# Optimization experiments

Hardware: AMD Instinct MI355X
Metric: run time of the kernel (lower is better)

## Reference

```python
import jax, jax.numpy as jnp
import numpy as np

N_NODES = 10000
N_EDGES = 320000
NEG_SLOPE = 0.2  # PyG GATConv default leaky_relu slope
EPS = 1e-16      # PyG softmax denominator epsilon


def setup_inputs() -> dict:
    key = jax.random.key(0)
    ks = jax.random.split(key, 9)
    x = jax.random.normal(ks[0], (N_NODES, 128), dtype=jnp.float32)
    edge_index = jax.random.randint(ks[1], (2, N_EDGES), 0, N_NODES, dtype=jnp.int64)
    W1 = jax.random.normal(ks[2], (128, 320), dtype=jnp.float32) * 0.05
    att_src1 = jax.random.normal(ks[3], (5, 64), dtype=jnp.float32) * 0.1
    att_dst1 = jax.random.normal(ks[4], (5, 64), dtype=jnp.float32) * 0.1
    b1 = jnp.zeros((320,), dtype=jnp.float32)
    W2 = jax.random.normal(ks[5], (320, 64), dtype=jnp.float32) * 0.05
    att_src2 = jax.random.normal(ks[6], (1, 64), dtype=jnp.float32) * 0.1
    att_dst2 = jax.random.normal(ks[7], (1, 64), dtype=jnp.float32) * 0.1
    b2 = jnp.zeros((64,), dtype=jnp.float32)
    return {"x": x, "edge_index": edge_index, "W1": W1, "att_src1": att_src1,
            "att_dst1": att_dst1, "b1": b1, "W2": W2, "att_src2": att_src2,
            "att_dst2": att_dst2, "b2": b2}


def gat_conv(x, src, dst, W, att_src, att_dst, bias, heads, out_c, concat):
    """PyG-style GATConv (eval mode, self-loops already in src/dst)."""
    N = x.shape[0]
    h = (x @ W).reshape(N, heads, out_c)                 # [N, H, C]
    a_src = jnp.einsum('nhc,hc->nh', h, att_src)         # [N, H]
    a_dst = jnp.einsum('nhc,hc->nh', h, att_dst)         # [N, H]
    e = a_src[src] + a_dst[dst]                          # [E, H]
    e = jax.nn.leaky_relu(e, NEG_SLOPE)
    # segment softmax over incoming edges of each destination node
    m = jax.ops.segment_max(e, dst, num_segments=N)      # [N, H]
    ex = jnp.exp(e - m[dst])
    s = jax.ops.segment_sum(ex, dst, num_segments=N)     # [N, H]
    alpha = ex / (s[dst] + EPS)                          # [E, H]
    out = jax.ops.segment_sum(h[src] * alpha[:, :, None], dst, num_segments=N)
    if concat:
        out = out.reshape(N, heads * out_c)
    else:
        out = out.mean(axis=1)
    return out + bias


def reference(x, edge_index, W1, att_src1, att_dst1, b1, W2, att_src2, att_dst2, b2):
    N = x.shape[0]
    loop = jnp.arange(N, dtype=edge_index.dtype)
    src = jnp.concatenate([edge_index[0], loop])  # add self-loops (PyG default)
    dst = jnp.concatenate([edge_index[1], loop])
    h = jax.nn.relu(gat_conv(x, src, dst, W1, att_src1, att_dst1, b1, 5, 64, True))
    h = jax.nn.relu(gat_conv(h, src, dst, W2, att_src2, att_dst2, b2, 1, 64, False))
    # F.dropout with training=False is identity (eval mode)
    return h
```

## Files before the change

kernel.cpp:

```cpp
#include <hip/hip_runtime.h>
#include <math.h>

#define N_NODES 10000
#define N_EDGES 320000
#define ET (N_EDGES + N_NODES)
#define CAP 128
#define NB_G1 (157 * 5)
#define NB_SCT ((ET + 255) / 256)

__device__ __forceinline__ float lrelu_exp(float e) {
  e = (e > 0.f) ? e : 0.2f * e;
  return __expf(e);
}


__global__ __launch_bounds__(256) void k_init(int* __restrict__ cursor) {
  int i = blockIdx.x * 256 + threadIdx.x;
  if (i < N_NODES) cursor[i] = 0;
}


__global__ __launch_bounds__(256) void k_gemm1_scatter(const float* __restrict__ x, const float* __restrict__ W1,
                                                       const float* __restrict__ att_src, const float* __restrict__ att_dst,
                                                       float* __restrict__ h1, float* __restrict__ a_src,
                                                       float* __restrict__ a_dst,
                                                       const int* __restrict__ ei, int* __restrict__ cursor,
                                                       int* __restrict__ csr) {
  __shared__ float xs[128][65];
  int bid = blockIdx.x;
  int t = threadIdx.x;
  if (bid >= NB_G1) {
    int i = (bid - NB_G1) * 256 + t;
    if (i < ET) {
      int src, dst;
      if (i < N_EDGES) { src = ei[i]; dst = ei[N_EDGES + i]; }
      else             { src = dst = i - N_EDGES; }
      int pos = (dst << 7) + atomicAdd(&cursor[dst], 1);
      csr[pos] = src;
    }
    return;
  }
  int h = bid / 157;
  int rb = (bid % 157) * 64;
#pragma unroll
  for (int i = 0; i < 8; ++i) {
    int idx = t + 256 * i;
    int kq = (idx & 31) * 4;
    int row = idx >> 5;
    int gr = rb + row;
    float4 v = make_float4(0.f, 0.f, 0.f, 0.f);
    if (gr < N_NODES) v = *reinterpret_cast<const float4*>(&x[(size_t)gr * 128 + kq]);
    xs[kq + 0][row] = v.x; xs[kq + 1][row] = v.y; xs[kq + 2][row] = v.z; xs[kq + 3][row] = v.w;
  }
  __syncthreads();
  int cg = t & 15, rg = t >> 4;
  int c0 = cg * 4, r0 = rg * 4;
  const float* __restrict__ wp = W1 + h * 64 + c0;
  float4 a0 = make_float4(0.f,0.f,0.f,0.f), a1 = a0, a2 = a0, a3 = a0;
#pragma unroll 4
  for (int k = 0; k < 128; ++k) {
    float4 xv = *reinterpret_cast<const float4*>(&xs[k][r0]);
    float4 wv = *reinterpret_cast<const float4*>(&wp[(size_t)k * 320]);
    a0.x = fmaf(xv.x, wv.x, a0.x); a0.y = fmaf(xv.x, wv.y, a0.y); a0.z = fmaf(xv.x, wv.z, a0.z); a0.w = fmaf(xv.x, wv.w, a0.w);
    a1.x = fmaf(xv.y, wv.x, a1.x); a1.y = fmaf(xv.y, wv.y, a1.y); a1.z = fmaf(xv.y, wv.z, a1.z); a1.w = fmaf(xv.y, wv.w, a1.w);
    a2.x = fmaf(xv.z, wv.x, a2.x); a2.y = fmaf(xv.z, wv.y, a2.y); a2.z = fmaf(xv.z, wv.z, a2.z); a2.w = fmaf(xv.z, wv.w, a2.w);
    a3.x = fmaf(xv.w, wv.x, a3.x); a3.y = fmaf(xv.w, wv.y, a3.y); a3.z = fmaf(xv.w, wv.z, a3.z); a3.w = fmaf(xv.w, wv.w, a3.w);
  }
  float4 asv = *reinterpret_cast<const float4*>(&att_src[h * 64 + c0]);
  float4 adv = *reinterpret_cast<const float4*>(&att_dst[h * 64 + c0]);
#pragma unroll
  for (int rr = 0; rr < 4; ++rr) {
    float4 ar = (rr == 0) ? a0 : (rr == 1) ? a1 : (rr == 2) ? a2 : a3;
    float vs = ar.x * asv.x + ar.y * asv.y + ar.z * asv.z + ar.w * asv.w;
    float vd = ar.x * adv.x + ar.y * adv.y + ar.z * adv.z + ar.w * adv.w;
#pragma unroll
    for (int m = 1; m < 16; m <<= 1) { vs += __shfl_xor(vs, m); vd += __shfl_xor(vd, m); }
    int gr = rb + r0 + rr;
    if (gr < N_NODES) {
      if (cg == 0) { a_src[h * N_NODES + gr] = vs; a_dst[h * N_NODES + gr] = vd; }
      *reinterpret_cast<float4*>(&h1[(size_t)gr * 320 + h * 64 + c0]) = ar;
    }
  }
}


__global__ __launch_bounds__(256) void k_agg1(const float* __restrict__ h1, const float* __restrict__ a_src,
                                              const float* __restrict__ a_dst, const float* __restrict__ b1,
                                              const int* __restrict__ degs, const int* __restrict__ csr,
                                              float* __restrict__ out1) {
  int lane = threadIdx.x & 63, wid = threadIdx.x >> 6;
  int n = blockIdx.x * 4 + wid;
  int h = blockIdx.y;
  int sub = lane >> 4;
  int cq = lane & 15;
  int beg = n << 7;
  int deg = degs[n];
  int limit = beg + deg;
  int end = beg + ((deg + 15) & ~15);
  const float* __restrict__ as = a_src + (size_t)h * N_NODES;
  float adn = a_dst[(size_t)h * N_NODES + n];
  const float* __restrict__ hh = h1 + h * 64 + cq * 4;
  float4 acc = make_float4(0.f, 0.f, 0.f, 0.f);
  float s = 0.f;
  int e = beg + sub;
  bool va = e < limit, vb = e + 4 < limit, vc = e + 8 < limit, vd = e + 12 < limit;
  int t0 = csr[e], t1 = csr[e + 4], t2 = csr[e + 8], t3 = csr[e + 12];
  unsigned i0 = va ? (unsigned)t0 : 0u, i1 = vb ? (unsigned)t1 : 0u;
  unsigned i2 = vc ? (unsigned)t2 : 0u, i3 = vd ? (unsigned)t3 : 0u;
  float v0 = as[i0], v1 = as[i1], v2 = as[i2], v3 = as[i3];
  for (;;) {
    float4 ga = *reinterpret_cast<const float4*>(hh + i0 * 320u);
    float4 gb = *reinterpret_cast<const float4*>(hh + i1 * 320u);
    float4 gc = *reinterpret_cast<const float4*>(hh + i2 * 320u);
    float4 gd = *reinterpret_cast<const float4*>(hh + i3 * 320u);
    float pa = va ? lrelu_exp(v0 + adn) : 0.f;
    float pb = vb ? lrelu_exp(v1 + adn) : 0.f;
    float pc = vc ? lrelu_exp(v2 + adn) : 0.f;
    float pd = vd ? lrelu_exp(v3 + adn) : 0.f;
    e += 16;
    bool more = e < end;
    if (more) {
      va = e < limit; vb = e + 4 < limit; vc = e + 8 < limit; vd = e + 12 < limit;
      t0 = csr[e]; t1 = csr[e + 4]; t2 = csr[e + 8]; t3 = csr[e + 12];
      i0 = va ? (unsigned)t0 : 0u; i1 = vb ? (unsigned)t1 : 0u;
      i2 = vc ? (unsigned)t2 : 0u; i3 = vd ? (unsigned)t3 : 0u;
      v0 = as[i0]; v1 = as[i1]; v2 = as[i2]; v3 = as[i3];
    }
    s += (pa + pb) + (pc + pd);
    acc.x = fmaf(pd, gd.x, fmaf(pc, gc.x, fmaf(pb, gb.x, fmaf(pa, ga.x, acc.x))));
    acc.y = fmaf(pd, gd.y, fmaf(pc, gc.y, fmaf(pb, gb.y, fmaf(pa, ga.y, acc.y))));
    acc.z = fmaf(pd, gd.z, fmaf(pc, gc.z, fmaf(pb, gb.z, fmaf(pa, ga.z, acc.z))));
    acc.w = fmaf(pd, gd.w, fmaf(pc, gc.w, fmaf(pb, gb.w, fmaf(pa, ga.w, acc.w))));
    if (!more) break;
  }
#pragma unroll
  for (int m = 16; m <= 32; m <<= 1) {
    acc.x += __shfl_xor(acc.x, m);
    acc.y += __shfl_xor(acc.y, m);
    acc.z += __shfl_xor(acc.z, m);
    acc.w += __shfl_xor(acc.w, m);
    s += __shfl_xor(s, m);
  }
  if (sub == 0) {
    float inv = 1.f / (s + 1e-16f);
    const float* bp = b1 + h * 64 + cq * 4;
    float4 o;
    o.x = fmaxf(fmaf(acc.x, inv, bp[0]), 0.f);
    o.y = fmaxf(fmaf(acc.y, inv, bp[1]), 0.f);
    o.z = fmaxf(fmaf(acc.z, inv, bp[2]), 0.f);
    o.w = fmaxf(fmaf(acc.w, inv, bp[3]), 0.f);
    *reinterpret_cast<float4*>(&out1[(size_t)n * 320 + h * 64 + cq * 4]) = o;
  }
}

__global__ __launch_bounds__(256) void k_agg2(const float* __restrict__ h2, const float* __restrict__ a_src,
                                              const float* __restrict__ a_dst, const float* __restrict__ b2,
                                              const int* __restrict__ degs, const int* __restrict__ csr,
                                              float* __restrict__ out) {
  int lane = threadIdx.x & 63, wid = threadIdx.x >> 6;
  int n = blockIdx.x * 4 + wid;
  int sub = lane >> 4;
  int cq = lane & 15;
  int beg = n << 7;
  int deg = degs[n];
  int limit = beg + deg;
  int end = beg + ((deg + 15) & ~15);
  float adn = a_dst[n];
  const float* __restrict__ hh = h2 + cq * 4;
  float4 acc = make_float4(0.f, 0.f, 0.f, 0.f);
  float s = 0.f;
  int e = beg + sub;
  bool va = e < limit, vb = e + 4 < limit, vc = e + 8 < limit, vd = e + 12 < limit;
  int t0 = csr[e], t1 = csr[e + 4], t2 = csr[e + 8], t3 = csr[e + 12];
  unsigned i0 = va ? (unsigned)t0 : 0u, i1 = vb ? (unsigned)t1 : 0u;
  unsigned i2 = vc ? (unsigned)t2 : 0u, i3 = vd ? (unsigned)t3 : 0u;
  float v0 = a_src[i0], v1 = a_src[i1], v2 = a_src[i2], v3 = a_src[i3];
  for (;;) {
    float4 ga = *reinterpret_cast<const float4*>(hh + i0 * 64u);
    float4 gb = *reinterpret_cast<const float4*>(hh + i1 * 64u);
    float4 gc = *reinterpret_cast<const float4*>(hh + i2 * 64u);
    float4 gd = *reinterpret_cast<const float4*>(hh + i3 * 64u);
    float pa = va ? lrelu_exp(v0 + adn) : 0.f;
    float pb = vb ? lrelu_exp(v1 + adn) : 0.f;
    float pc = vc ? lrelu_exp(v2 + adn) : 0.f;
    float pd = vd ? lrelu_exp(v3 + adn) : 0.f;
    e += 16;
    bool more = e < end;
    if (more) {
      va = e < limit; vb = e + 4 < limit; vc = e + 8 < limit; vd = e + 12 < limit;
      t0 = csr[e]; t1 = csr[e + 4]; t2 = csr[e + 8]; t3 = csr[e + 12];
      i0 = va ? (unsigned)t0 : 0u; i1 = vb ? (unsigned)t1 : 0u;
      i2 = vc ? (unsigned)t2 : 0u; i3 = vd ? (unsigned)t3 : 0u;
      v0 = a_src[i0]; v1 = a_src[i1]; v2 = a_src[i2]; v3 = a_src[i3];
    }
    s += (pa + pb) + (pc + pd);
    acc.x = fmaf(pd, gd.x, fmaf(pc, gc.x, fmaf(pb, gb.x, fmaf(pa, ga.x, acc.x))));
    acc.y = fmaf(pd, gd.y, fmaf(pc, gc.y, fmaf(pb, gb.y, fmaf(pa, ga.y, acc.y))));
    acc.z = fmaf(pd, gd.z, fmaf(pc, gc.z, fmaf(pb, gb.z, fmaf(pa, ga.z, acc.z))));
    acc.w = fmaf(pd, gd.w, fmaf(pc, gc.w, fmaf(pb, gb.w, fmaf(pa, ga.w, acc.w))));
    if (!more) break;
  }
#pragma unroll
  for (int m = 16; m <= 32; m <<= 1) {
    acc.x += __shfl_xor(acc.x, m);
    acc.y += __shfl_xor(acc.y, m);
    acc.z += __shfl_xor(acc.z, m);
    acc.w += __shfl_xor(acc.w, m);
    s += __shfl_xor(s, m);
  }
  if (sub == 0) {
    float inv = 1.f / (s + 1e-16f);
    const float* bp = b2 + cq * 4;
    float4 o;
    o.x = fmaxf(fmaf(acc.x, inv, bp[0]), 0.f);
    o.y = fmaxf(fmaf(acc.y, inv, bp[1]), 0.f);
    o.z = fmaxf(fmaf(acc.z, inv, bp[2]), 0.f);
    o.w = fmaxf(fmaf(acc.w, inv, bp[3]), 0.f);
    *reinterpret_cast<float4*>(&out[(size_t)n * 64 + cq * 4]) = o;
  }
}


__global__ __launch_bounds__(256) void k_gemm2(const float* __restrict__ out1, const float* __restrict__ W2,
                                               float* __restrict__ h2part) {
  __shared__ float xs[64][65];
  int t = threadIdx.x;
  int rb = blockIdx.x * 64;
  int kc = blockIdx.y;
#pragma unroll
  for (int i = 0; i < 4; ++i) {
    int idx = t + 256 * i;
    int kq = (idx & 15) * 4;
    int row = idx >> 4;
    int gr = rb + row;
    float4 v = make_float4(0.f, 0.f, 0.f, 0.f);
    if (gr < N_NODES) v = *reinterpret_cast<const float4*>(&out1[(size_t)gr * 320 + kc * 64 + kq]);
    xs[kq + 0][row] = v.x; xs[kq + 1][row] = v.y; xs[kq + 2][row] = v.z; xs[kq + 3][row] = v.w;
  }
  __syncthreads();
  int cg = t & 15, rg = t >> 4;
  int c0 = cg * 4, r0 = rg * 4;
  const float* __restrict__ wp = W2 + (size_t)kc * 64 * 64 + c0;
  float4 a0 = make_float4(0.f,0.f,0.f,0.f), a1 = a0, a2 = a0, a3 = a0;
#pragma unroll 4
  for (int k = 0; k < 64; ++k) {
    float4 xv = *reinterpret_cast<const float4*>(&xs[k][r0]);
    float4 wv = *reinterpret_cast<const float4*>(&wp[(size_t)k * 64]);
    a0.x = fmaf(xv.x, wv.x, a0.x); a0.y = fmaf(xv.x, wv.y, a0.y); a0.z = fmaf(xv.x, wv.z, a0.z); a0.w = fmaf(xv.x, wv.w, a0.w);
    a1.x = fmaf(xv.y, wv.x, a1.x); a1.y = fmaf(xv.y, wv.y, a1.y); a1.z = fmaf(xv.y, wv.z, a1.z); a1.w = fmaf(xv.y, wv.w, a1.w);
    a2.x = fmaf(xv.z, wv.x, a2.x); a2.y = fmaf(xv.z, wv.y, a2.y); a2.z = fmaf(xv.z, wv.z, a2.z); a2.w = fmaf(xv.z, wv.w, a2.w);
    a3.x = fmaf(xv.w, wv.x, a3.x); a3.y = fmaf(xv.w, wv.y, a3.y); a3.z = fmaf(xv.w, wv.z, a3.z); a3.w = fmaf(xv.w, wv.w, a3.w);
  }
  float* __restrict__ hp = h2part + (size_t)kc * N_NODES * 64;
#pragma unroll
  for (int rr = 0; rr < 4; ++rr) {
    float4 ar = (rr == 0) ? a0 : (rr == 1) ? a1 : (rr == 2) ? a2 : a3;
    int gr = rb + r0 + rr;
    if (gr < N_NODES) *reinterpret_cast<float4*>(&hp[(size_t)gr * 64 + c0]) = ar;
  }
}


__global__ __launch_bounds__(256) void k_hred2(const float* __restrict__ h2part,
                                               const float* __restrict__ att_src, const float* __restrict__ att_dst,
                                               float* __restrict__ h2, float* __restrict__ a_src,
                                               float* __restrict__ a_dst) {
  int n = blockIdx.x * 4 + (threadIdx.x >> 6);
  int c = threadIdx.x & 63;
  if (n >= N_NODES) return;
  float v = 0.f;
#pragma unroll
  for (int kc = 0; kc < 5; ++kc) v += h2part[((size_t)kc * N_NODES + n) * 64 + c];
  float vs = v * att_src[c], vd = v * att_dst[c];
  for (int off = 32; off; off >>= 1) {
    vs += __shfl_down(vs, off);
    vd += __shfl_down(vd, off);
  }
  h2[(size_t)n * 64 + c] = v;
  if (c == 0) { a_src[n] = vs; a_dst[n] = vd; }
}


extern "C" void kernel_launch(void* const* d_in, const int* in_sizes, int n_in,
                              void* d_out, int out_size, void* d_ws, size_t ws_size,
                              hipStream_t stream) {
  (void)in_sizes; (void)n_in; (void)out_size; (void)ws_size;
  const float* x    = (const float*)d_in[0];
  const int*   ei   = (const int*)d_in[1];
  const float* W1   = (const float*)d_in[2];
  const float* as1w = (const float*)d_in[3];
  const float* ad1w = (const float*)d_in[4];
  const float* b1   = (const float*)d_in[5];
  const float* W2   = (const float*)d_in[6];
  const float* as2w = (const float*)d_in[7];
  const float* ad2w = (const float*)d_in[8];
  const float* b2   = (const float*)d_in[9];
  float* out = (float*)d_out;

  char* ws = (char*)d_ws;
  size_t off = 0;
  auto alloc = [&](size_t bytes) -> void* {
    void* p = ws + off;
    off += (bytes + 255) & ~(size_t)255;
    return p;
  };
  float*  h1     = (float*)alloc((size_t)N_NODES * 320 * 4);
  float*  out1   = (float*)alloc((size_t)N_NODES * 320 * 4);
  float*  h2     = (float*)alloc((size_t)N_NODES * 64 * 4);
  float*  h2part = (float*)alloc((size_t)5 * N_NODES * 64 * 4);
  float*  a_src1 = (float*)alloc((size_t)5 * N_NODES * 4);
  float*  a_dst1 = (float*)alloc((size_t)5 * N_NODES * 4);
  float*  a_src2 = (float*)alloc((size_t)N_NODES * 4);
  float*  a_dst2 = (float*)alloc((size_t)N_NODES * 4);
  int*    cursor = (int*)alloc((size_t)N_NODES * 4);
  int*    csr    = (int*)alloc((size_t)N_NODES * CAP * 4);

  k_init<<<(N_NODES + 255) / 256, 256, 0, stream>>>(cursor);
  k_gemm1_scatter<<<NB_G1 + NB_SCT, 256, 0, stream>>>(x, W1, as1w, ad1w, h1, a_src1, a_dst1,
                                                      ei, cursor, csr);
  {
    dim3 g(N_NODES / 4, 5);
    k_agg1 <<<g, 256, 0, stream>>>(h1, a_src1, a_dst1, b1, cursor, csr, out1);
  }
  {
    dim3 g((N_NODES + 63) / 64, 5);
    k_gemm2<<<g, 256, 0, stream>>>(out1, W2, h2part);
  }
  k_hred2<<<(N_NODES + 3) / 4, 256, 0, stream>>>(h2part, as2w, ad2w, h2, a_src2, a_dst2);
  k_agg2 <<<N_NODES / 4, 256, 0, stream>>>(h2, a_src2, a_dst2, b2, cursor, csr, out);
}
```

Measured before the change: 103.4 us.

## Fuse second-layer GEMM with attention-score reduction, dropping split-K partials

```diff
diff --git a/kernel.cpp b/kernel.cpp
--- a/kernel.cpp
+++ b/kernel.cpp
@@ -222,62 +222,44 @@
 
 
 __global__ __launch_bounds__(256) void k_gemm2(const float* __restrict__ out1, const float* __restrict__ W2,
-                                               float* __restrict__ h2part) {
-  __shared__ float xs[64][65];
-  int t = threadIdx.x;
-  int rb = blockIdx.x * 64;
-  int kc = blockIdx.y;
-#pragma unroll
-  for (int i = 0; i < 4; ++i) {
-    int idx = t + 256 * i;
-    int kq = (idx & 15) * 4;
-    int row = idx >> 4;
-    int gr = rb + row;
-    float4 v = make_float4(0.f, 0.f, 0.f, 0.f);
-    if (gr < N_NODES) v = *reinterpret_cast<const float4*>(&out1[(size_t)gr * 320 + kc * 64 + kq]);
-    xs[kq + 0][row] = v.x; xs[kq + 1][row] = v.y; xs[kq + 2][row] = v.z; xs[kq + 3][row] = v.w;
-  }
-  __syncthreads();
-  int cg = t & 15, rg = t >> 4;
-  int c0 = cg * 4, r0 = rg * 4;
-  const float* __restrict__ wp = W2 + (size_t)kc * 64 * 64 + c0;
-  float4 a0 = make_float4(0.f,0.f,0.f,0.f), a1 = a0, a2 = a0, a3 = a0;
-#pragma unroll 4
-  for (int k = 0; k < 64; ++k) {
-    float4 xv = *reinterpret_cast<const float4*>(&xs[k][r0]);
-    float4 wv = *reinterpret_cast<const float4*>(&wp[(size_t)k * 64]);
-    a0.x = fmaf(xv.x, wv.x, a0.x); a0.y = fmaf(xv.x, wv.y, a0.y); a0.z = fmaf(xv.x, wv.z, a0.z); a0.w = fmaf(xv.x, wv.w, a0.w);
-    a1.x = fmaf(xv.y, wv.x, a1.x); a1.y = fmaf(xv.y, wv.y, a1.y); a1.z = fmaf(xv.y, wv.z, a1.z); a1.w = fmaf(xv.y, wv.w, a1.w);
-    a2.x = fmaf(xv.z, wv.x, a2.x); a2.y = fmaf(xv.z, wv.y, a2.y); a2.z = fmaf(xv.z, wv.z, a2.z); a2.w = fmaf(xv.z, wv.w, a2.w);
-    a3.x = fmaf(xv.w, wv.x, a3.x); a3.y = fmaf(xv.w, wv.y, a3.y); a3.z = fmaf(xv.w, wv.z, a3.z); a3.w = fmaf(xv.w, wv.w, a3.w);
-  }
-  float* __restrict__ hp = h2part + (size_t)kc * N_NODES * 64;
-#pragma unroll
-  for (int rr = 0; rr < 4; ++rr) {
-    float4 ar = (rr == 0) ? a0 : (rr == 1) ? a1 : (rr == 2) ? a2 : a3;
-    int gr = rb + r0 + rr;
-    if (gr < N_NODES) *reinterpret_cast<float4*>(&hp[(size_t)gr * 64 + c0]) = ar;
-  }
-}
-
-
-__global__ __launch_bounds__(256) void k_hred2(const float* __restrict__ h2part,
                                                const float* __restrict__ att_src, const float* __restrict__ att_dst,
                                                float* __restrict__ h2, float* __restrict__ a_src,
                                                float* __restrict__ a_dst) {
-  int n = blockIdx.x * 4 + (threadIdx.x >> 6);
-  int c = threadIdx.x & 63;
-  if (n >= N_NODES) return;
-  float v = 0.f;
-#pragma unroll
-  for (int kc = 0; kc < 5; ++kc) v += h2part[((size_t)kc * N_NODES + n) * 64 + c];
-  float vs = v * att_src[c], vd = v * att_dst[c];
-  for (int off = 32; off; off >>= 1) {
-    vs += __shfl_down(vs, off);
-    vd += __shfl_down(vd, off);
-  }
-  h2[(size_t)n * 64 + c] = v;
-  if (c == 0) { a_src[n] = vs; a_dst[n] = vd; }
+  __shared__ float xs[16][320];
+  int t = threadIdx.x;
+  int rb = blockIdx.x * 16;
+#pragma unroll
+  for (int i = 0; i < 5; ++i) {
+    int idx = t + 256 * i;
+    int row = idx / 80;
+    int kq = (idx - row * 80) * 4;
+    float4 v = *reinterpret_cast<const float4*>(&out1[(size_t)(rb + row) * 320 + kq]);
+    *reinterpret_cast<float4*>(&xs[row][kq]) = v;
+  }
+  __syncthreads();
+  int lane = t & 63, wid = t >> 6;
+  int r0 = wid * 4;
+  float acc0 = 0.f, acc1 = 0.f, acc2 = 0.f, acc3 = 0.f;
+  const float* __restrict__ wp = W2 + lane;
+#pragma unroll 4
+  for (int k = 0; k < 320; ++k) {
+    float w = wp[(size_t)k * 64];
+    acc0 = fmaf(xs[r0 + 0][k], w, acc0);
+    acc1 = fmaf(xs[r0 + 1][k], w, acc1);
+    acc2 = fmaf(xs[r0 + 2][k], w, acc2);
+    acc3 = fmaf(xs[r0 + 3][k], w, acc3);
+  }
+  float as = att_src[lane], ad = att_dst[lane];
+#pragma unroll
+  for (int rr = 0; rr < 4; ++rr) {
+    float a = (rr == 0) ? acc0 : (rr == 1) ? acc1 : (rr == 2) ? acc2 : acc3;
+    float vs = a * as, vd = a * ad;
+#pragma unroll
+    for (int m = 1; m < 64; m <<= 1) { vs += __shfl_xor(vs, m); vd += __shfl_xor(vd, m); }
+    int gr = rb + r0 + rr;
+    h2[(size_t)gr * 64 + lane] = a;
+    if (lane == 0) { a_src[gr] = vs; a_dst[gr] = vd; }
+  }
 }
 
 
@@ -307,7 +289,6 @@
   float*  h1     = (float*)alloc((size_t)N_NODES * 320 * 4);
   float*  out1   = (float*)alloc((size_t)N_NODES * 320 * 4);
   float*  h2     = (float*)alloc((size_t)N_NODES * 64 * 4);
-  float*  h2part = (float*)alloc((size_t)5 * N_NODES * 64 * 4);
   float*  a_src1 = (float*)alloc((size_t)5 * N_NODES * 4);
   float*  a_dst1 = (float*)alloc((size_t)5 * N_NODES * 4);
   float*  a_src2 = (float*)alloc((size_t)N_NODES * 4);
@@ -322,10 +303,6 @@
     dim3 g(N_NODES / 4, 5);
     k_agg1 <<<g, 256, 0, stream>>>(h1, a_src1, a_dst1, b1, cursor, csr, out1);
   }
-  {
-    dim3 g((N_NODES + 63) / 64, 5);
-    k_gemm2<<<g, 256, 0, stream>>>(out1, W2, h2part);
-  }
-  k_hred2<<<(N_NODES + 3) / 4, 256, 0, stream>>>(h2part, as2w, ad2w, h2, a_src2, a_dst2);
+  k_gemm2<<<N_NODES / 16, 256, 0, stream>>>(out1, W2, as2w, ad2w, h2, a_src2, a_dst2);
   k_agg2 <<<N_NODES / 4, 256, 0, stream>>>(h2, a_src2, a_dst2, b2, cursor, csr, out);
 }
```

After: 111.5 us. +7.9%, slower.
